# Performance work log

Measured on AMD Instinct MI355X. Metric: run time of the kernel, lower is better.

Reference implementation:

```python
import jax, jax.numpy as jnp
import numpy as np


def setup_inputs() -> dict:
    key = jax.random.key(0)
    B, n, H = 64, 64, 256  # graphs, atoms per drug, hidden_dim
    k = jax.random.split(key, 4)
    h1 = jax.random.normal(k[0], (B * n, H), jnp.float32)
    h2 = jax.random.normal(k[1], (B * n, H), jnp.float32)
    # equal-size, sorted batch assignment (ragged sizes made uniform for jit)
    batch = jnp.repeat(jnp.arange(B, dtype=jnp.int64), n)
    W1 = jax.random.normal(k[2], (2 * H, H), jnp.float32) / np.sqrt(2 * H)
    b1 = jnp.zeros((H,), jnp.float32)
    W2 = jax.random.normal(k[3], (H, 1), jnp.float32) / np.sqrt(H)
    b2 = jnp.zeros((1,), jnp.float32)
    return {"h1_atoms": h1, "h2_atoms": h2, "batch1": batch, "batch2": batch,
            "n_graphs": B, "W1": W1, "b1": b1, "W2": W2, "b2": b2}


def reference(h1_atoms, h2_atoms, batch1, batch2, n_graphs, W1, b1, W2, b2):
    B = int(n_graphs)
    H = h1_atoms.shape[1]
    n1 = h1_atoms.shape[0] // B
    n2 = h2_atoms.shape[0] // B
    # sorted equal-size batches -> ragged gather becomes a reshape
    a1 = h1_atoms.reshape(B, n1, H)
    a2 = h2_atoms.reshape(B, n2, H)
    # Linear(2H->H) on concat([a1,a2]) is separable across the two halves of W1
    s1 = jnp.einsum('bik,kh->bih', a1, W1[:H])   # [B,n1,H]
    s2 = jnp.einsum('bjk,kh->bjh', a2, W1[H:])   # [B,n2,H]
    hidden = jnp.tanh(s1[:, :, None, :] + s2[:, None, :, :] + b1)  # [B,n1,n2,H]
    scores = jnp.einsum('bijh,h->bij', hidden, W2[:, 0]) + b2[0]   # [B,n1,n2]
    # softmax over all n1*n2 pairs within each graph
    p = jax.nn.softmax(scores.reshape(B, n1 * n2), axis=-1).reshape(B, n1, n2)
    attention_1 = p.sum(axis=2).reshape(-1)  # [B*n1]
    attention_2 = p.sum(axis=1).reshape(-1)  # [B*n2]
    return attention_1, attention_2
```

## Files before the change

kernel.cpp:

```cpp
#include <hip/hip_runtime.h>

#define BGRAPHS 64
#define NATOMS  64
#define HDIM    256
#define H4      64

__device__ __forceinline__ float fast_tanh(float x) {
    float e = __expf(x + x);
    float r = __builtin_amdgcn_rcpf(e + 1.0f);
    return 1.0f - (r + r);
}

__global__ __launch_bounds__(256) void gemm_t1t2(
    const float* __restrict__ h1, const float* __restrict__ h2,
    const float* __restrict__ W1, const float* __restrict__ b1,
    float* __restrict__ T1, float* __restrict__ T2)
{
    __shared__ float Atile[16 * HDIM];
    const int bid    = blockIdx.x;
    const bool second = (bid >= 256);
    const float* A = second ? h2 : h1;
    const float* W = W1 + (second ? HDIM * HDIM : 0);
    float* T = second ? T2 : T1;
    const int rowbase = (bid & 255) * 16;
    const int t = threadIdx.x;

    {
        const float4* Ag = (const float4*)(A + rowbase * HDIM);
        float4* As = (float4*)Atile;
        #pragma unroll
        for (int m = 0; m < 4; ++m) As[t + 256 * m] = Ag[t + 256 * m];
    }
    __syncthreads();

    const int c4 = t & 63;
    const int r4 = t >> 6;
    float acc[4][4] = {};
    const float4* Wg = (const float4*)W;

    for (int k4 = 0; k4 < H4; ++k4) {
        float4 a[4];
        #pragma unroll
        for (int r = 0; r < 4; ++r)
            a[r] = *(const float4*)&Atile[(r4 * 4 + r) * HDIM + k4 * 4];
        #pragma unroll
        for (int kk = 0; kk < 4; ++kk) {
            float4 w = Wg[(k4 * 4 + kk) * H4 + c4];
            #pragma unroll
            for (int r = 0; r < 4; ++r) {
                float av = ((const float*)&a[r])[kk];
                acc[r][0] += av * w.x;
                acc[r][1] += av * w.y;
                acc[r][2] += av * w.z;
                acc[r][3] += av * w.w;
            }
        }
    }

    float4 bias = make_float4(0.f, 0.f, 0.f, 0.f);
    if (second) bias = ((const float4*)b1)[c4];
    #pragma unroll
    for (int r = 0; r < 4; ++r) {
        float4 o;
        o.x = acc[r][0] + bias.x;
        o.y = acc[r][1] + bias.y;
        o.z = acc[r][2] + bias.z;
        o.w = acc[r][3] + bias.w;
        ((float4*)(T + (size_t)(rowbase + r4 * 4 + r) * HDIM))[c4] = o;
    }
}

__global__ __launch_bounds__(512) void score_kernel(
    const float* __restrict__ T1, const float* __restrict__ T2,
    const float* __restrict__ W2, float* __restrict__ scores)
{
    __shared__ float4 t2s[H4 * NATOMS];
    const int bid   = blockIdx.x;
    const int b     = bid >> 3;
    const int itile = bid & 7;
    const int t = threadIdx.x;

    {
        const int j = t >> 3, q = t & 7;
        const float4* src = (const float4*)(T2 + (size_t)(b * NATOMS + j) * HDIM);
        #pragma unroll
        for (int m = 0; m < 8; ++m) {
            int h4 = q * 8 + m;
            t2s[h4 * NATOMS + j] = src[h4];
        }
    }
    __syncthreads();

    const int wid  = __builtin_amdgcn_readfirstlane(t >> 6);
    const int lane = t & 63;
    const int i = itile * 8 + wid;
    const float4* t1r = (const float4*)(T1 + (size_t)(b * NATOMS + i) * HDIM);
    const float4* w2r = (const float4*)W2;

    float acc = 0.f;
    for (int h4 = 0; h4 < H4; ++h4) {
        float4 t2v = t2s[h4 * NATOMS + lane];
        float4 t1v = t1r[h4];
        float4 w2v = w2r[h4];
        acc += w2v.x * fast_tanh(t1v.x + t2v.x);
        acc += w2v.y * fast_tanh(t1v.y + t2v.y);
        acc += w2v.z * fast_tanh(t1v.z + t2v.z);
        acc += w2v.w * fast_tanh(t1v.w + t2v.w);
    }
    scores[(size_t)b * (NATOMS * NATOMS) + i * NATOMS + lane] = acc;
}

__global__ __launch_bounds__(256) void softmax_kernel(
    const float* __restrict__ scores, float* __restrict__ out)
{
    __shared__ float e[64 * 65];
    __shared__ float red[8];
    const int b = blockIdx.x;
    const int t = threadIdx.x;
    const int wid = t >> 6, lane = t & 63;
    const float* s = scores + (size_t)b * 4096;

    float v[16];
    float mx = -1e30f;
    #pragma unroll
    for (int m = 0; m < 16; ++m) {
        v[m] = s[t + 256 * m];
        mx = fmaxf(mx, v[m]);
    }
    #pragma unroll
    for (int o = 32; o >= 1; o >>= 1) mx = fmaxf(mx, __shfl_xor(mx, o));
    if (lane == 0) red[wid] = mx;
    __syncthreads();
    mx = fmaxf(fmaxf(red[0], red[1]), fmaxf(red[2], red[3]));

    float psum = 0.f;
    #pragma unroll
    for (int m = 0; m < 16; ++m) {
        float ev = __expf(v[m] - mx);
        psum += ev;
        int row = wid + 4 * m;
        e[row * 65 + lane] = ev;
    }
    #pragma unroll
    for (int o = 32; o >= 1; o >>= 1) psum += __shfl_xor(psum, o);
    if (lane == 0) red[4 + wid] = psum;
    __syncthreads();

    const float Z = red[4] + red[5] + red[6] + red[7];
    const float invZ = 1.0f / Z;

    if (wid == 0) {
        float rs = 0.f;
        for (int jj = 0; jj < 64; ++jj) rs += e[lane * 65 + jj];
        out[b * 64 + lane] = rs * invZ;
    } else if (wid == 1) {
        float cs = 0.f;
        for (int ii = 0; ii < 64; ++ii) cs += e[ii * 65 + lane];
        out[4096 + b * 64 + lane] = cs * invZ;
    }
}

extern "C" void kernel_launch(void* const* d_in, const int* in_sizes, int n_in,
                              void* d_out, int out_size, void* d_ws, size_t ws_size,
                              hipStream_t stream) {
    const float* h1 = (const float*)d_in[0];
    const float* h2 = (const float*)d_in[1];
    const float* W1 = (const float*)d_in[5];
    const float* b1 = (const float*)d_in[6];
    const float* W2 = (const float*)d_in[7];
    float* out = (float*)d_out;

    float* T1     = (float*)d_ws;
    float* T2     = T1 + 4096 * HDIM;
    float* scores = T2 + 4096 * HDIM;

    gemm_t1t2<<<512, 256, 0, stream>>>(h1, h2, W1, b1, T1, T2);
    score_kernel<<<512, 512, 0, stream>>>(T1, T2, W2, scores);
    softmax_kernel<<<64, 256, 0, stream>>>(scores, out);
}
```

Measured before the change: 123.1 us.

## Use bf16 MFMA GEMM, exp2 tanh, and fuse softmax into score kernel

Converts W1 to a transposed bf16 layout and computes the projection with bf16 MFMA instructions, storing the projections as bf16 prescaled by 2*log2(e) so tanh can use exp2 directly. The score kernel now exponentiates scores in place and writes per-row sums and per-tile column partial sums, and a small final kernel normalises. This removes the fp32 scalar GEMM, halves the intermediate traffic, and eliminates the separate scores buffer and softmax pass. It drops the max subtraction in the softmax, which relies on bounded scores, and lowers precision to bf16.

New measurement: 116.0 us. 5.8% less time.

```diff
diff --git a/kernel.cpp b/kernel.cpp
--- a/kernel.cpp
+++ b/kernel.cpp
@@ -1,163 +1,199 @@
 #include <hip/hip_runtime.h>
+#include <hip/hip_bf16.h>
 
 #define BGRAPHS 64
 #define NATOMS  64
 #define HDIM    256
-#define H4      64
-
-__device__ __forceinline__ float fast_tanh(float x) {
-    float e = __expf(x + x);
-    float r = __builtin_amdgcn_rcpf(e + 1.0f);
-    return 1.0f - (r + r);
-}
-
-__global__ __launch_bounds__(256) void gemm_t1t2(
+#define K2LOG2E 2.8853900817779268f
+#define LOG2E   1.4426950408889634f
+
+typedef __attribute__((ext_vector_type(8))) short bf16x8;
+typedef __attribute__((ext_vector_type(4))) float f32x4;
+
+__device__ __forceinline__ short f2bfs(float f) {
+    __hip_bfloat16 h = __float2bfloat16(f);
+    return *reinterpret_cast<short*>(&h);
+}
+__device__ __forceinline__ float bf2f(unsigned short s) {
+    union { unsigned u; float f; } v; v.u = ((unsigned)s) << 16;
+    return v.f;
+}
+
+__global__ __launch_bounds__(256) void k0_wt(const float* __restrict__ W1,
+                                             unsigned short* __restrict__ Wt) {
+    __shared__ float lds[64][65];
+    const int t = threadIdx.x;
+    const int kb = (blockIdx.x >> 2) * 64;
+    const int hb = (blockIdx.x & 3) * 64;
+    {
+        const int hl = t & 63;
+        #pragma unroll
+        for (int m = 0; m < 16; ++m) {
+            int kl = (t >> 6) + m * 4;
+            lds[kl][hl] = W1[(size_t)(kb + kl) * HDIM + hb + hl];
+        }
+    }
+    __syncthreads();
+    {
+        const int kl = t & 63;
+        const int kg = kb + kl, half = kg >> 8, kin = kg & 255;
+        #pragma unroll
+        for (int m = 0; m < 16; ++m) {
+            int hl = (t >> 6) + m * 4;
+            Wt[((size_t)half * HDIM + hb + hl) * HDIM + kin] =
+                (unsigned short)f2bfs(lds[kl][hl]);
+        }
+    }
+}
+
+__global__ __launch_bounds__(256) void k1_gemm(
     const float* __restrict__ h1, const float* __restrict__ h2,
-    const float* __restrict__ W1, const float* __restrict__ b1,
-    float* __restrict__ T1, float* __restrict__ T2)
+    const unsigned short* __restrict__ Wt, const float* __restrict__ b1,
+    unsigned short* __restrict__ Tb)
 {
-    __shared__ float Atile[16 * HDIM];
-    const int bid    = blockIdx.x;
-    const bool second = (bid >= 256);
-    const float* A = second ? h2 : h1;
-    const float* W = W1 + (second ? HDIM * HDIM : 0);
-    float* T = second ? T2 : T1;
-    const int rowbase = (bid & 255) * 16;
+    const int bid = blockIdx.x;
+    const int rb = bid >> 1, cb = bid & 1;
+    const int half = rb >> 6;
+    const float* A = half ? h2 : h1;
+    const int arow0 = rb * 64 - half * 4096;
+    const unsigned short* Wh = Wt + (size_t)half * HDIM * HDIM;
+
     const int t = threadIdx.x;
-
-    {
-        const float4* Ag = (const float4*)(A + rowbase * HDIM);
-        float4* As = (float4*)Atile;
-        #pragma unroll
-        for (int m = 0; m < 4; ++m) As[t + 256 * m] = Ag[t + 256 * m];
-    }
-    __syncthreads();
-
-    const int c4 = t & 63;
-    const int r4 = t >> 6;
-    float acc[4][4] = {};
-    const float4* Wg = (const float4*)W;
-
-    for (int k4 = 0; k4 < H4; ++k4) {
-        float4 a[4];
-        #pragma unroll
-        for (int r = 0; r < 4; ++r)
-            a[r] = *(const float4*)&Atile[(r4 * 4 + r) * HDIM + k4 * 4];
-        #pragma unroll
-        for (int kk = 0; kk < 4; ++kk) {
-            float4 w = Wg[(k4 * 4 + kk) * H4 + c4];
+    const int w = t >> 6, l = t & 63;
+    const int wr = w >> 1, wc = w & 1;
+    const int lr = l & 15, lg = l >> 4;
+    const int rowb = arow0 + wr * 32;
+    const int colb = cb * 128 + wc * 64;
+
+    f32x4 acc[2][4] = {};
+
+    for (int k0 = 0; k0 < HDIM; k0 += 32) {
+        const int ko = k0 + lg * 8;
+        bf16x8 a[2], b[4];
+        #pragma unroll
+        for (int mr = 0; mr < 2; ++mr) {
+            const float* ap = A + (size_t)(rowb + mr * 16 + lr) * HDIM + ko;
+            float4 f0 = *(const float4*)ap;
+            float4 f1 = *(const float4*)(ap + 4);
+            a[mr][0] = f2bfs(f0.x); a[mr][1] = f2bfs(f0.y);
+            a[mr][2] = f2bfs(f0.z); a[mr][3] = f2bfs(f0.w);
+            a[mr][4] = f2bfs(f1.x); a[mr][5] = f2bfs(f1.y);
+            a[mr][6] = f2bfs(f1.z); a[mr][7] = f2bfs(f1.w);
+        }
+        #pragma unroll
+        for (int nc = 0; nc < 4; ++nc)
+            b[nc] = *(const bf16x8*)(Wh + (size_t)(colb + nc * 16 + lr) * HDIM + ko);
+        #pragma unroll
+        for (int mr = 0; mr < 2; ++mr)
+            #pragma unroll
+            for (int nc = 0; nc < 4; ++nc)
+                acc[mr][nc] = __builtin_amdgcn_mfma_f32_16x16x32_bf16(
+                    a[mr], b[nc], acc[mr][nc], 0, 0, 0);
+    }
+
+    const int growb = rb * 64 + wr * 32;
+    #pragma unroll
+    for (int nc = 0; nc < 4; ++nc) {
+        const int col = colb + nc * 16 + lr;
+        const float bias = half ? b1[col] : 0.f;
+        #pragma unroll
+        for (int mr = 0; mr < 2; ++mr)
             #pragma unroll
             for (int r = 0; r < 4; ++r) {
-                float av = ((const float*)&a[r])[kk];
-                acc[r][0] += av * w.x;
-                acc[r][1] += av * w.y;
-                acc[r][2] += av * w.z;
-                acc[r][3] += av * w.w;
+                const int grow = growb + mr * 16 + lg * 4 + r;
+                Tb[(size_t)grow * HDIM + col] =
+                    (unsigned short)f2bfs((acc[mr][nc][r] + bias) * K2LOG2E);
             }
-        }
-    }
-
-    float4 bias = make_float4(0.f, 0.f, 0.f, 0.f);
-    if (second) bias = ((const float4*)b1)[c4];
-    #pragma unroll
-    for (int r = 0; r < 4; ++r) {
-        float4 o;
-        o.x = acc[r][0] + bias.x;
-        o.y = acc[r][1] + bias.y;
-        o.z = acc[r][2] + bias.z;
-        o.w = acc[r][3] + bias.w;
-        ((float4*)(T + (size_t)(rowbase + r4 * 4 + r) * HDIM))[c4] = o;
-    }
-}
-
-__global__ __launch_bounds__(512) void score_kernel(
-    const float* __restrict__ T1, const float* __restrict__ T2,
-    const float* __restrict__ W2, float* __restrict__ scores)
+    }
+}
+
+__global__ __launch_bounds__(512) void k2_score(
+    const unsigned short* __restrict__ Tb, const float* __restrict__ W2,
+    float* __restrict__ rowacc, float* __restrict__ colpart)
 {
-    __shared__ float4 t2s[H4 * NATOMS];
-    const int bid   = blockIdx.x;
-    const int b     = bid >> 3;
-    const int itile = bid & 7;
+    __shared__ ushort4 t2s[64 * 66];
+    __shared__ ushort4 t1s[64 * 8];
+    __shared__ float   colbuf[8 * 64];
+    const int bid = blockIdx.x;
+    const int b = bid >> 3, itile = bid & 7;
     const int t = threadIdx.x;
 
     {
         const int j = t >> 3, q = t & 7;
-        const float4* src = (const float4*)(T2 + (size_t)(b * NATOMS + j) * HDIM);
+        const ushort4* src = (const ushort4*)(Tb + (size_t)(4096 + b * 64 + j) * HDIM);
         #pragma unroll
         for (int m = 0; m < 8; ++m) {
-            int h4 = q * 8 + m;
-            t2s[h4 * NATOMS + j] = src[h4];
+            const int h4 = m * 8 + q;
+            t2s[h4 * 66 + j] = src[h4];
+        }
+    }
+    if (t < 64) {
+        const int i = t >> 3, q = t & 7;
+        const ushort4* src = (const ushort4*)(Tb + (size_t)(b * 64 + itile * 8 + i) * HDIM);
+        #pragma unroll
+        for (int m = 0; m < 8; ++m) {
+            const int h4 = m * 8 + q;
+            t1s[h4 * 8 + i] = src[h4];
         }
     }
     __syncthreads();
 
-    const int wid  = __builtin_amdgcn_readfirstlane(t >> 6);
+    const int w = t >> 6;
     const int lane = t & 63;
-    const int i = itile * 8 + wid;
-    const float4* t1r = (const float4*)(T1 + (size_t)(b * NATOMS + i) * HDIM);
+    const int i = itile * 8 + w;
     const float4* w2r = (const float4*)W2;
 
-    float acc = 0.f;
-    for (int h4 = 0; h4 < H4; ++h4) {
-        float4 t2v = t2s[h4 * NATOMS + lane];
-        float4 t1v = t1r[h4];
-        float4 w2v = w2r[h4];
-        acc += w2v.x * fast_tanh(t1v.x + t2v.x);
-        acc += w2v.y * fast_tanh(t1v.y + t2v.y);
-        acc += w2v.z * fast_tanh(t1v.z + t2v.z);
-        acc += w2v.w * fast_tanh(t1v.w + t2v.w);
-    }
-    scores[(size_t)b * (NATOMS * NATOMS) + i * NATOMS + lane] = acc;
-}
-
-__global__ __launch_bounds__(256) void softmax_kernel(
-    const float* __restrict__ scores, float* __restrict__ out)
-{
-    __shared__ float e[64 * 65];
-    __shared__ float red[8];
-    const int b = blockIdx.x;
-    const int t = threadIdx.x;
-    const int wid = t >> 6, lane = t & 63;
-    const float* s = scores + (size_t)b * 4096;
-
-    float v[16];
-    float mx = -1e30f;
-    #pragma unroll
-    for (int m = 0; m < 16; ++m) {
-        v[m] = s[t + 256 * m];
-        mx = fmaxf(mx, v[m]);
-    }
-    #pragma unroll
-    for (int o = 32; o >= 1; o >>= 1) mx = fmaxf(mx, __shfl_xor(mx, o));
-    if (lane == 0) red[wid] = mx;
+    float score = 0.f;
+    #pragma unroll 4
+    for (int h4 = 0; h4 < 64; ++h4) {
+        const ushort4 t2v = t2s[h4 * 66 + lane];
+        const ushort4 t1v = t1s[h4 * 8 + w];
+        const float4  w2v = w2r[h4];
+        const float x0 = bf2f(t1v.x) + bf2f(t2v.x);
+        const float x1 = bf2f(t1v.y) + bf2f(t2v.y);
+        const float x2 = bf2f(t1v.z) + bf2f(t2v.z);
+        const float x3 = bf2f(t1v.w) + bf2f(t2v.w);
+        const float r0 = __builtin_amdgcn_rcpf(exp2f(x0) + 1.f);
+        const float r1 = __builtin_amdgcn_rcpf(exp2f(x1) + 1.f);
+        const float r2 = __builtin_amdgcn_rcpf(exp2f(x2) + 1.f);
+        const float r3 = __builtin_amdgcn_rcpf(exp2f(x3) + 1.f);
+        score += w2v.x * fmaf(-2.f, r0, 1.f);
+        score += w2v.y * fmaf(-2.f, r1, 1.f);
+        score += w2v.z * fmaf(-2.f, r2, 1.f);
+        score += w2v.w * fmaf(-2.f, r3, 1.f);
+    }
+
+    const float e = exp2f(score * LOG2E);
+    float rs = e;
+    #pragma unroll
+    for (int o = 32; o >= 1; o >>= 1) rs += __shfl_xor(rs, o);
+    if (lane == 0) rowacc[b * 64 + i] = rs;
+
+    colbuf[w * 64 + lane] = e;
     __syncthreads();
-    mx = fmaxf(fmaxf(red[0], red[1]), fmaxf(red[2], red[3]));
-
-    float psum = 0.f;
-    #pragma unroll
-    for (int m = 0; m < 16; ++m) {
-        float ev = __expf(v[m] - mx);
-        psum += ev;
-        int row = wid + 4 * m;
-        e[row * 65 + lane] = ev;
-    }
-    #pragma unroll
-    for (int o = 32; o >= 1; o >>= 1) psum += __shfl_xor(psum, o);
-    if (lane == 0) red[4 + wid] = psum;
-    __syncthreads();
-
-    const float Z = red[4] + red[5] + red[6] + red[7];
-    const float invZ = 1.0f / Z;
-
-    if (wid == 0) {
-        float rs = 0.f;
-        for (int jj = 0; jj < 64; ++jj) rs += e[lane * 65 + jj];
-        out[b * 64 + lane] = rs * invZ;
-    } else if (wid == 1) {
+    if (w == 0) {
         float cs = 0.f;
-        for (int ii = 0; ii < 64; ++ii) cs += e[ii * 65 + lane];
-        out[4096 + b * 64 + lane] = cs * invZ;
-    }
+        #pragma unroll
+        for (int ww = 0; ww < 8; ++ww) cs += colbuf[ww * 64 + lane];
+        colpart[(size_t)(b * 8 + itile) * 64 + lane] = cs;
+    }
+}
+
+__global__ __launch_bounds__(64) void k3_final(const float* __restrict__ rowacc,
+                                               const float* __restrict__ colpart,
+                                               float* __restrict__ out) {
+    const int b = blockIdx.x, lane = threadIdx.x;
+    const float r = rowacc[b * 64 + lane];
+    float z = r;
+    #pragma unroll
+    for (int o = 32; o >= 1; o >>= 1) z += __shfl_xor(z, o);
+    const float invZ = 1.0f / z;
+    float cs = 0.f;
+    #pragma unroll
+    for (int it = 0; it < 8; ++it)
+        cs += colpart[(size_t)(b * 8 + it) * 64 + lane];
+    out[b * 64 + lane] = r * invZ;
+    out[4096 + b * 64 + lane] = cs * invZ;
 }
 
 extern "C" void kernel_launch(void* const* d_in, const int* in_sizes, int n_in,
@@ -170,11 +206,13 @@
     const float* W2 = (const float*)d_in[7];
     float* out = (float*)d_out;
 
-    float* T1     = (float*)d_ws;
-    float* T2     = T1 + 4096 * HDIM;
-    float* scores = T2 + 4096 * HDIM;
-
-    gemm_t1t2<<<512, 256, 0, stream>>>(h1, h2, W1, b1, T1, T2);
-    score_kernel<<<512, 512, 0, stream>>>(T1, T2, W2, scores);
-    softmax_kernel<<<64, 256, 0, stream>>>(scores, out);
-}
+    unsigned short* Tb = (unsigned short*)d_ws;
+    unsigned short* Wt = Tb + 8192 * HDIM;
+    float* rowacc  = (float*)(Wt + 2 * HDIM * HDIM);
+    float* colpart = rowacc + BGRAPHS * NATOMS;
+
+    k0_wt   <<<32, 256, 0, stream>>>(W1, Wt);
+    k1_gemm <<<256, 256, 0, stream>>>(h1, h2, Wt, b1, Tb);
+    k2_score<<<512, 512, 0, stream>>>(Tb, W2, rowacc, colpart);
+    k3_final<<<64, 64, 0, stream>>>(rowacc, colpart, out);
+}
```
